# Performance work log

Hardware: AMD Instinct MI355X
Metric: run time of the kernel (lower is better)

Reference implementation:

```python
import jax, jax.numpy as jnp
import numpy as np

BN_EPS = 1e-5


def setup_inputs() -> dict:
    key = jax.random.key(0)
    k1, k2 = jax.random.split(key)
    B, IN, OUT = 8192, 4096, 4096
    x = jax.random.normal(k1, (B, IN), dtype=jnp.float32)
    weight = jax.random.normal(k2, (OUT, IN), dtype=jnp.float32) * 0.1
    bias = jnp.zeros((OUT,), dtype=jnp.float32)
    return {"x": x, "weight": weight, "bias": bias}


def reference(x, weight, bias):
    # Binarize activations and weights to {-1, 0, +1} via sign (sign(0)=0, matching torch).
    bx = jnp.sign(x)            # [B, IN]
    bw = jnp.sign(weight)       # [OUT, IN]
    out = jnp.einsum('bi,oi->bo', bx, bw) + bias  # F.linear
    # BatchNorm1d, training mode, affine=False: normalize with batch mean / biased var.
    mean = jnp.mean(out, axis=0)
    var = jnp.mean(jnp.square(out - mean), axis=0)
    return (out - mean) * jax.lax.rsqrt(var + BN_EPS)
```

## Files before the change

kernel.cpp:

```cpp
#include <hip/hip_runtime.h>
#include <stdint.h>

#define B_ROWS 8192
#define IN_DIM 4096
#define OUT_DIM 4096
#define BN_EPS 1e-5f

#define TILE 128
#define BK 64
#define NKCH (IN_DIM / BK)

typedef __attribute__((ext_vector_type(4))) int i32x4;

__device__ __forceinline__ int sign_byte(float f) {
    int s = (f > 0.f) ? 1 : ((f < 0.f) ? -1 : 0);
    return s & 0xFF;
}

__global__ void pack_i8(const float* __restrict__ in, int* __restrict__ out) {
    int gid = blockIdx.x * blockDim.x + threadIdx.x;
    float4 v = reinterpret_cast<const float4*>(in)[gid];
    out[gid] = sign_byte(v.x) | (sign_byte(v.y) << 8) |
               (sign_byte(v.z) << 16) | (sign_byte(v.w) << 24);
}

__global__ __launch_bounds__(256) void bin_gemm_i8(
    const int8_t* __restrict__ A,
    const int8_t* __restrict__ W,
    float* __restrict__ out,
    float* __restrict__ colsum,
    float* __restrict__ colsumsq)
{
    __shared__ i32x4 a_sm4[TILE * BK / 16];
    __shared__ i32x4 b_sm4[TILE * BK / 16];
    __shared__ float s_sum[TILE];
    __shared__ float s_sq[TILE];

    int8_t* a_sm = reinterpret_cast<int8_t*>(a_sm4);
    int8_t* b_sm = reinterpret_cast<int8_t*>(b_sm4);

    const int t      = threadIdx.x;
    const int lane   = t & 63;
    const int wave   = t >> 6;
    const int wr     = wave >> 1;
    const int wc     = wave & 1;
    const int lane16 = lane & 15;
    const int quad   = lane >> 4;
    const int row0   = blockIdx.y * TILE;
    const int col0   = blockIdx.x * TILE;

    if (t < TILE) { s_sum[t] = 0.f; s_sq[t] = 0.f; }

    i32x4 acc[4][4] = {};

    const int8_t* src  = (wave < 2) ? A : W;
    const int     gbase = (wave < 2) ? row0 : col0;
    int8_t*       dst  = (wave < 2) ? a_sm : b_sm;
    const int     half = (wave & 1) * 64;
    const int     lrow = lane >> 2;
    const int     slot = lane & 3;

    for (int ch = 0; ch < NKCH; ++ch) {
        const int k0 = ch * BK;
        __syncthreads();
#pragma unroll
        for (int p = 0; p < 4; ++p) {
            int row = half + p * 16 + lrow;
            int g   = slot ^ ((row >> 1) & 3);
            const int8_t* gp = src + (size_t)(gbase + row) * IN_DIM + k0 + g * 16;
            int8_t* lp = dst + (half + p * 16) * BK + lane * 16;
            __builtin_amdgcn_global_load_lds(
                (const __attribute__((address_space(1))) void*)gp,
                (__attribute__((address_space(3))) void*)lp, 16, 0, 0);
        }
        __syncthreads();

        i32x4 af[4], bf[4];
#pragma unroll
        for (int i = 0; i < 4; ++i) {
            int row = wr * 64 + i * 16 + lane16;
            int s   = quad ^ ((row >> 1) & 3);
            af[i] = *reinterpret_cast<const i32x4*>(a_sm + row * BK + s * 16);
        }
#pragma unroll
        for (int j = 0; j < 4; ++j) {
            int col = wc * 64 + j * 16 + lane16;
            int s   = quad ^ ((col >> 1) & 3);
            bf[j] = *reinterpret_cast<const i32x4*>(b_sm + col * BK + s * 16);
        }
#pragma unroll
        for (int i = 0; i < 4; ++i)
#pragma unroll
            for (int j = 0; j < 4; ++j)
                acc[i][j] = __builtin_amdgcn_mfma_i32_16x16x64_i8(
                    af[i], bf[j], acc[i][j], 0, 0, 0);
    }

    float csum[4] = {0.f, 0.f, 0.f, 0.f};
    float csq[4]  = {0.f, 0.f, 0.f, 0.f};
#pragma unroll
    for (int i = 0; i < 4; ++i) {
#pragma unroll
        for (int r = 0; r < 4; ++r) {
            int grow = row0 + wr * 64 + i * 16 + quad * 4 + r;
            float* orow = out + (size_t)grow * OUT_DIM + col0 + wc * 64 + lane16;
#pragma unroll
            for (int j = 0; j < 4; ++j) {
                float v = (float)acc[i][j][r];
                orow[j * 16] = v;
                csum[j] += v;
                csq[j]  += v * v;
            }
        }
    }
#pragma unroll
    for (int j = 0; j < 4; ++j) {
        csum[j] += __shfl_xor(csum[j], 16);
        csum[j] += __shfl_xor(csum[j], 32);
        csq[j]  += __shfl_xor(csq[j], 16);
        csq[j]  += __shfl_xor(csq[j], 32);
    }
    if (quad == 0) {
#pragma unroll
        for (int j = 0; j < 4; ++j) {
            atomicAdd(&s_sum[wc * 64 + j * 16 + lane16], csum[j]);
            atomicAdd(&s_sq [wc * 64 + j * 16 + lane16], csq[j]);
        }
    }
    __syncthreads();
    if (t < TILE) {
        atomicAdd(&colsum[col0 + t],   s_sum[t]);
        atomicAdd(&colsumsq[col0 + t], s_sq[t]);
    }
}

__global__ void bn_stats(const float* __restrict__ colsum,
                         const float* __restrict__ colsumsq,
                         float* __restrict__ mean, float* __restrict__ rstd) {
    int o = blockIdx.x * blockDim.x + threadIdx.x;
    float m = colsum[o] * (1.0f / B_ROWS);
    float v = colsumsq[o] * (1.0f / B_ROWS) - m * m;
    mean[o] = m;
    rstd[o] = rsqrtf(v + BN_EPS);
}

__global__ void bn_apply(float* __restrict__ out,
                         const float* __restrict__ mean,
                         const float* __restrict__ rstd) {
    size_t f = (size_t)blockIdx.x * blockDim.x + threadIdx.x;
    int c4 = (int)(f & (OUT_DIM / 4 - 1));
    float4 v = reinterpret_cast<float4*>(out)[f];
    float4 m = reinterpret_cast<const float4*>(mean)[c4];
    float4 r = reinterpret_cast<const float4*>(rstd)[c4];
    v.x = (v.x - m.x) * r.x;
    v.y = (v.y - m.y) * r.y;
    v.z = (v.z - m.z) * r.z;
    v.w = (v.w - m.w) * r.w;
    reinterpret_cast<float4*>(out)[f] = v;
}

extern "C" void kernel_launch(void* const* d_in, const int* in_sizes, int n_in,
                              void* d_out, int out_size, void* d_ws, size_t ws_size,
                              hipStream_t stream) {
    const float* x = (const float*)d_in[0];
    const float* w = (const float*)d_in[1];
    float* out = (float*)d_out;

    uint8_t* ws = (uint8_t*)d_ws;
    int8_t* xb = (int8_t*)ws;
    int8_t* wb = (int8_t*)(ws + (size_t)B_ROWS * IN_DIM);
    float* colsum   = (float*)(ws + (size_t)B_ROWS * IN_DIM
                                  + (size_t)OUT_DIM * IN_DIM);
    float* colsumsq = colsum + OUT_DIM;
    float* mean     = colsumsq + OUT_DIM;
    float* rstd     = mean + OUT_DIM;

    hipMemsetAsync(colsum, 0, 2 * OUT_DIM * sizeof(float), stream);

    pack_i8<<<(B_ROWS * IN_DIM / 4) / 256, 256, 0, stream>>>(x, (int*)xb);
    pack_i8<<<(OUT_DIM * IN_DIM / 4) / 256, 256, 0, stream>>>(w, (int*)wb);

    bin_gemm_i8<<<dim3(OUT_DIM / TILE, B_ROWS / TILE), 256, 0, stream>>>(
        xb, wb, out, colsum, colsumsq);

    bn_stats<<<OUT_DIM / 256, 256, 0, stream>>>(colsum, colsumsq, mean, rstd);

    bn_apply<<<(unsigned)((size_t)B_ROWS * OUT_DIM / 4 / 256), 256, 0, stream>>>(
        out, mean, rstd);
}
```

Measured before the change: 449.1 us.

## Rewrite int8 GEMM with 256x256 tiles, double-buffered LDS and phased MFMA schedule

Replaces the 128x128, BK=64 single-buffered GEMM with a 512-thread, 256x256-tile kernel that uses BK=128 and a two-stage LDS double buffer. Global-to-LDS loads are interleaved with MFMA phases using explicit barriers, waitcnt and setprio, and the block index is swizzled for L2 locality. The aim is to hide load latency and raise arithmetic intensity on the GEMM that dominates runtime. In exchange it uses 128KB of LDS and a large accumulator array, and relies on fragile hand-tuned waitcnt counts.

```diff
diff --git a/kernel.cpp b/kernel.cpp
--- a/kernel.cpp
+++ b/kernel.cpp
@@ -6,9 +6,11 @@
 #define OUT_DIM 4096
 #define BN_EPS 1e-5f
 
-#define TILE 128
-#define BK 64
-#define NKCH (IN_DIM / BK)
+#define BM 256
+#define BLKN 256
+#define BKB 128
+#define NKT (IN_DIM / BKB)
+#define NIT (NKT / 2)
 
 typedef __attribute__((ext_vector_type(4))) int i32x4;
 
@@ -24,111 +26,208 @@
                (sign_byte(v.z) << 16) | (sign_byte(v.w) << 24);
 }
 
-__global__ __launch_bounds__(256) void bin_gemm_i8(
+__device__ __forceinline__ void stage_pair(const int8_t* g0, int8_t* l0) {
+    __builtin_amdgcn_global_load_lds(
+        (const __attribute__((address_space(1))) void*)g0,
+        (__attribute__((address_space(3))) void*)l0, 16, 0, 0);
+    __builtin_amdgcn_global_load_lds(
+        (const __attribute__((address_space(1))) void*)(g0 + (size_t)128 * IN_DIM),
+        (__attribute__((address_space(3))) void*)(l0 + 128 * BKB), 16, 0, 0);
+}
+
+template <int FB>
+__device__ __forceinline__ void load_frag4(i32x4 d[4][2], const int8_t* base,
+                                           int off0, int off1) {
+#pragma unroll
+    for (int f = 0; f < 4; ++f) {
+        d[f][0] = *reinterpret_cast<const i32x4*>(base + (FB + f) * (16 * BKB) + off0);
+        d[f][1] = *reinterpret_cast<const i32x4*>(base + (FB + f) * (16 * BKB) + off1);
+    }
+}
+
+template <int FB>
+__device__ __forceinline__ void load_frag2(i32x4 d[2][2], const int8_t* base,
+                                           int off0, int off1) {
+#pragma unroll
+    for (int f = 0; f < 2; ++f) {
+        d[f][0] = *reinterpret_cast<const i32x4*>(base + (FB + f) * (16 * BKB) + off0);
+        d[f][1] = *reinterpret_cast<const i32x4*>(base + (FB + f) * (16 * BKB) + off1);
+    }
+}
+
+template <int AM, int AN>
+__device__ __forceinline__ void mfma_quad(i32x4 acc[8][4], const i32x4 a[4][2],
+                                          const i32x4 b[2][2]) {
+#pragma unroll
+    for (int mf = 0; mf < 4; ++mf)
+#pragma unroll
+        for (int nf = 0; nf < 2; ++nf) {
+            acc[AM + mf][AN + nf] = __builtin_amdgcn_mfma_i32_16x16x64_i8(
+                a[mf][0], b[nf][0], acc[AM + mf][AN + nf], 0, 0, 0);
+            acc[AM + mf][AN + nf] = __builtin_amdgcn_mfma_i32_16x16x64_i8(
+                a[mf][1], b[nf][1], acc[AM + mf][AN + nf], 0, 0, 0);
+        }
+}
+
+#define PHASE_MID()                                             \
+    __builtin_amdgcn_s_barrier();                               \
+    asm volatile("s_waitcnt lgkmcnt(0)" ::: "memory");          \
+    __builtin_amdgcn_sched_barrier(0);                          \
+    __builtin_amdgcn_s_setprio(1)
+
+#define PHASE_END()                                             \
+    __builtin_amdgcn_s_setprio(0);                              \
+    __builtin_amdgcn_s_barrier()
+
+#define PHASE_END_VM()                                          \
+    __builtin_amdgcn_s_setprio(0);                              \
+    asm volatile("s_waitcnt vmcnt(6)" ::: "memory");            \
+    __builtin_amdgcn_s_barrier()
+
+__global__ __launch_bounds__(512, 2) void bin_gemm_i8(
     const int8_t* __restrict__ A,
     const int8_t* __restrict__ W,
     float* __restrict__ out,
     float* __restrict__ colsum,
     float* __restrict__ colsumsq)
 {
-    __shared__ i32x4 a_sm4[TILE * BK / 16];
-    __shared__ i32x4 b_sm4[TILE * BK / 16];
-    __shared__ float s_sum[TILE];
-    __shared__ float s_sq[TILE];
-
-    int8_t* a_sm = reinterpret_cast<int8_t*>(a_sm4);
-    int8_t* b_sm = reinterpret_cast<int8_t*>(b_sm4);
+    __shared__ __align__(16) int8_t lds[2][2][BM * BKB];
+    __shared__ float s_sum[BLKN];
+    __shared__ float s_sq[BLKN];
 
     const int t      = threadIdx.x;
     const int lane   = t & 63;
     const int wave   = t >> 6;
-    const int wr     = wave >> 1;
-    const int wc     = wave & 1;
+    const int wm     = wave >> 2;
+    const int wn     = wave & 3;
     const int lane16 = lane & 15;
     const int quad   = lane >> 4;
-    const int row0   = blockIdx.y * TILE;
-    const int col0   = blockIdx.x * TILE;
-
-    if (t < TILE) { s_sum[t] = 0.f; s_sq[t] = 0.f; }
-
-    i32x4 acc[4][4] = {};
-
-    const int8_t* src  = (wave < 2) ? A : W;
-    const int     gbase = (wave < 2) ? row0 : col0;
-    int8_t*       dst  = (wave < 2) ? a_sm : b_sm;
-    const int     half = (wave & 1) * 64;
-    const int     lrow = lane >> 2;
-    const int     slot = lane & 3;
-
-    for (int ch = 0; ch < NKCH; ++ch) {
-        const int k0 = ch * BK;
-        __syncthreads();
-#pragma unroll
-        for (int p = 0; p < 4; ++p) {
-            int row = half + p * 16 + lrow;
-            int g   = slot ^ ((row >> 1) & 3);
-            const int8_t* gp = src + (size_t)(gbase + row) * IN_DIM + k0 + g * 16;
-            int8_t* lp = dst + (half + p * 16) * BK + lane * 16;
-            __builtin_amdgcn_global_load_lds(
-                (const __attribute__((address_space(1))) void*)gp,
-                (__attribute__((address_space(3))) void*)lp, 16, 0, 0);
-        }
-        __syncthreads();
-
-        i32x4 af[4], bf[4];
-#pragma unroll
-        for (int i = 0; i < 4; ++i) {
-            int row = wr * 64 + i * 16 + lane16;
-            int s   = quad ^ ((row >> 1) & 3);
-            af[i] = *reinterpret_cast<const i32x4*>(a_sm + row * BK + s * 16);
-        }
-#pragma unroll
-        for (int j = 0; j < 4; ++j) {
-            int col = wc * 64 + j * 16 + lane16;
-            int s   = quad ^ ((col >> 1) & 3);
-            bf[j] = *reinterpret_cast<const i32x4*>(b_sm + col * BK + s * 16);
-        }
-#pragma unroll
-        for (int i = 0; i < 4; ++i)
-#pragma unroll
-            for (int j = 0; j < 4; ++j)
-                acc[i][j] = __builtin_amdgcn_mfma_i32_16x16x64_i8(
-                    af[i], bf[j], acc[i][j], 0, 0, 0);
+
+    const int flat = blockIdx.y * gridDim.x + blockIdx.x;
+    const int swz  = (flat & 7) * (512 / 8) + (flat >> 3);
+    const int row0 = (swz >> 4) * BM;
+    const int col0 = (swz & 15) * BLKN;
+
+    if (t < BLKN) { s_sum[t] = 0.f; s_sq[t] = 0.f; }
+
+    const int r6 = t >> 3;
+    const int c8 = t & 7;
+    const int gslot = ((c8 ^ (r6 & 7)) << 4);
+    const int rA0 = r6;
+    const int rB0 = r6 + (r6 & 32);
+
+    const int8_t* pA = A + (size_t)(row0 + rA0) * IN_DIM + gslot;
+    const int8_t* pW = W + (size_t)(col0 + rB0) * IN_DIM + gslot;
+    int8_t* lA0 = &lds[0][0][rA0 * BKB + c8 * 16];
+    int8_t* lB0 = &lds[0][1][rB0 * BKB + c8 * 16];
+
+    const int sw   = lane & 7;
+    const int off0 = ((quad ^ sw) << 4);
+    const int off1 = (((4 + quad) ^ sw) << 4);
+    const int8_t* rA = &lds[0][0][(wm * 128 + lane16) * BKB];
+    const int8_t* rB = &lds[0][1][(wn * 64 + lane16) * BKB];
+
+    i32x4 acc[8][4] = {};
+    i32x4 alo[4][2], ahi[4][2], bb[2][2];
+
+    stage_pair(pA,                             lA0);
+    stage_pair(pA + (size_t)64 * IN_DIM,       lA0 + 64 * BKB);
+    stage_pair(pW,                             lB0);
+    stage_pair(pW + (size_t)32 * IN_DIM,       lB0 + 32 * BKB);
+    stage_pair(pA + BKB,                       lA0 + 65536);
+    stage_pair(pA + (size_t)64 * IN_DIM + BKB, lA0 + 65536 + 64 * BKB);
+    stage_pair(pW + BKB,                       lB0 + 65536);
+    asm volatile("s_waitcnt vmcnt(6)" ::: "memory");
+    __builtin_amdgcn_s_barrier();
+
+#pragma unroll 1
+    for (int it = 0; it < NIT; ++it) {
+        const int tc1 = (2 * it + 1) & (NKT - 1);
+        const int tn0 = (2 * it + 2) & (NKT - 1);
+        const int tn1 = (2 * it + 3) & (NKT - 1);
+
+        load_frag4<0>(alo, rA, off0, off1);
+        load_frag2<0>(bb, rB, off0, off1);
+        stage_pair(pW + (size_t)32 * IN_DIM + tc1 * BKB, lB0 + 65536 + 32 * BKB);
+        PHASE_MID();
+        mfma_quad<0, 0>(acc, alo, bb);
+        PHASE_END();
+
+        load_frag4<4>(ahi, rA, off0, off1);
+        stage_pair(pA + tn0 * BKB, lA0);
+        PHASE_MID();
+        mfma_quad<4, 0>(acc, ahi, bb);
+        PHASE_END();
+
+        load_frag2<2>(bb, rB, off0, off1);
+        stage_pair(pA + (size_t)64 * IN_DIM + tn0 * BKB, lA0 + 64 * BKB);
+        PHASE_MID();
+        mfma_quad<4, 2>(acc, ahi, bb);
+        PHASE_END();
+
+        stage_pair(pW + tn0 * BKB, lB0);
+        PHASE_MID();
+        mfma_quad<0, 2>(acc, alo, bb);
+        PHASE_END_VM();
+
+        load_frag4<0>(alo, rA + 65536, off0, off1);
+        load_frag2<0>(bb, rB + 65536, off0, off1);
+        stage_pair(pW + (size_t)32 * IN_DIM + tn0 * BKB, lB0 + 32 * BKB);
+        PHASE_MID();
+        mfma_quad<0, 0>(acc, alo, bb);
+        PHASE_END();
+
+        load_frag4<4>(ahi, rA + 65536, off0, off1);
+        stage_pair(pA + tn1 * BKB, lA0 + 65536);
+        PHASE_MID();
+        mfma_quad<4, 0>(acc, ahi, bb);
+        PHASE_END();
+
+        load_frag2<2>(bb, rB + 65536, off0, off1);
+        stage_pair(pA + (size_t)64 * IN_DIM + tn1 * BKB, lA0 + 65536 + 64 * BKB);
+        PHASE_MID();
+        mfma_quad<4, 2>(acc, ahi, bb);
+        PHASE_END();
+
+        stage_pair(pW + tn1 * BKB, lB0 + 65536);
+        PHASE_MID();
+        mfma_quad<0, 2>(acc, alo, bb);
+        PHASE_END_VM();
     }
 
     float csum[4] = {0.f, 0.f, 0.f, 0.f};
     float csq[4]  = {0.f, 0.f, 0.f, 0.f};
 #pragma unroll
-    for (int i = 0; i < 4; ++i) {
+    for (int mf = 0; mf < 8; ++mf) {
 #pragma unroll
         for (int r = 0; r < 4; ++r) {
-            int grow = row0 + wr * 64 + i * 16 + quad * 4 + r;
-            float* orow = out + (size_t)grow * OUT_DIM + col0 + wc * 64 + lane16;
-#pragma unroll
-            for (int j = 0; j < 4; ++j) {
-                float v = (float)acc[i][j][r];
-                orow[j * 16] = v;
-                csum[j] += v;
-                csq[j]  += v * v;
+            int grow = row0 + wm * 128 + mf * 16 + quad * 4 + r;
+            float* orow = out + (size_t)grow * OUT_DIM + col0 + wn * 64 + lane16;
+#pragma unroll
+            for (int nf = 0; nf < 4; ++nf) {
+                float v = (float)acc[mf][nf][r];
+                orow[nf * 16] = v;
+                csum[nf] += v;
+                csq[nf]  += v * v;
             }
         }
     }
 #pragma unroll
-    for (int j = 0; j < 4; ++j) {
-        csum[j] += __shfl_xor(csum[j], 16);
-        csum[j] += __shfl_xor(csum[j], 32);
-        csq[j]  += __shfl_xor(csq[j], 16);
-        csq[j]  += __shfl_xor(csq[j], 32);
+    for (int nf = 0; nf < 4; ++nf) {
+        csum[nf] += __shfl_xor(csum[nf], 16);
+        csum[nf] += __shfl_xor(csum[nf], 32);
+        csq[nf]  += __shfl_xor(csq[nf], 16);
+        csq[nf]  += __shfl_xor(csq[nf], 32);
     }
     if (quad == 0) {
 #pragma unroll
-        for (int j = 0; j < 4; ++j) {
-            atomicAdd(&s_sum[wc * 64 + j * 16 + lane16], csum[j]);
-            atomicAdd(&s_sq [wc * 64 + j * 16 + lane16], csq[j]);
+        for (int nf = 0; nf < 4; ++nf) {
+            atomicAdd(&s_sum[wn * 64 + nf * 16 + lane16], csum[nf]);
+            atomicAdd(&s_sq [wn * 64 + nf * 16 + lane16], csq[nf]);
         }
     }
     __syncthreads();
-    if (t < TILE) {
+    if (t < BLKN) {
         atomicAdd(&colsum[col0 + t],   s_sum[t]);
         atomicAdd(&colsumsq[col0 + t], s_sq[t]);
     }
@@ -180,7 +279,7 @@
     pack_i8<<<(B_ROWS * IN_DIM / 4) / 256, 256, 0, stream>>>(x, (int*)xb);
     pack_i8<<<(OUT_DIM * IN_DIM / 4) / 256, 256, 0, stream>>>(w, (int*)wb);
 
-    bin_gemm_i8<<<dim3(OUT_DIM / TILE, B_ROWS / TILE), 256, 0, stream>>>(
+    bin_gemm_i8<<<dim3(OUT_DIM / BLKN, B_ROWS / BM), 512, 0, stream>>>(
         xb, wb, out, colsum, colsumsq);
 
     bn_stats<<<OUT_DIM / 256, 256, 0, stream>>>(colsum, colsumsq, mean, rstd);
```

Measured after the change: 437.0 us. -2.7%, faster.
